# Kernel optimization log

Hardware: AMD Instinct MI355X
Metric: run time of the kernel (lower is better)

## Reference

```python
import jax, jax.numpy as jnp
import numpy as np

B, N, F0 = 256, 256, 128
LAYER_SIZES = [128, 128, 128]


def setup_inputs() -> dict:
    key = jax.random.key(0)
    ks = jax.random.split(key, 10)
    x = jax.random.normal(ks[0], (B, N, F0), dtype=jnp.float32)
    adj = jax.random.uniform(ks[1], (B, N, N), dtype=jnp.float32)
    adj = 0.5 * (adj + jnp.swapaxes(adj, -1, -2))  # symmetric weighted adjacency
    f0, f1, f2 = LAYER_SIZES
    W1 = jax.random.normal(ks[2], (f0, f1), dtype=jnp.float32) / np.sqrt(f0)
    b1 = jnp.zeros((f1,), dtype=jnp.float32)
    W2 = jax.random.normal(ks[3], (f1, f2), dtype=jnp.float32) / np.sqrt(f1)
    b2 = jnp.zeros((f2,), dtype=jnp.float32)
    Wr = jax.random.normal(ks[4], (2 * f2, f2), dtype=jnp.float32) / np.sqrt(2 * f2)
    br = jnp.zeros((f2,), dtype=jnp.float32)
    return {"x": x, "adj": adj, "W1": W1, "b1": b1, "W2": W2, "b2": b2, "Wr": Wr, "br": br}


def _normalize_adj(adj):
    # DenseGCNConv: set self-loops (diag=1), then D^{-1/2} (A+I) D^{-1/2} with deg clamped to >=1
    n = adj.shape[-1]
    eye = jnp.eye(n, dtype=adj.dtype)
    a = adj * (1.0 - eye) + eye
    d = jnp.maximum(a.sum(axis=-1), 1.0) ** -0.5  # [B, N]
    return d[..., :, None] * a * d[..., None, :]


def reference(x, adj, W1, b1, W2, b2, Wr, br):
    a = _normalize_adj(adj)  # same adj for both layers; normalization is identical per layer
    h = jnp.einsum("bnm,bmf->bnf", a, x @ W1) + b1  # DenseGCNConv layer 1
    h = jnp.einsum("bnm,bmf->bnf", a, h @ W2) + b2  # DenseGCNConv layer 2
    pooled = jnp.concatenate([h.mean(axis=1), h.max(axis=1)], axis=-1)  # [B, 2F]
    return pooled @ Wr + br  # [B, F]
```

## Files before the change

### kernel.cpp

```cpp
#include <hip/hip_runtime.h>
#include <cstddef>


typedef __attribute__((ext_vector_type(8))) short short8;
typedef __attribute__((ext_vector_type(4))) float f32x4;

static __device__ __forceinline__ unsigned short f2bf(float f) {
  unsigned int u = __float_as_uint(f);
  u += 0x7FFFu + ((u >> 16) & 1u);
  return (unsigned short)(u >> 16);
}

static __device__ __forceinline__ f32x4 mfma16(short8 a, short8 b, f32x4 c) {
  return __builtin_amdgcn_mfma_f32_16x16x32_bf16(a, b, c, 0, 0, 0);
}

static __device__ __forceinline__ short8 load_bfrag(const float* p) {
  float4 u = *reinterpret_cast<const float4*>(p);
  float4 v = *reinterpret_cast<const float4*>(p + 4);
  short8 f;
  f[0] = (short)f2bf(u.x); f[1] = (short)f2bf(u.y);
  f[2] = (short)f2bf(u.z); f[3] = (short)f2bf(u.w);
  f[4] = (short)f2bf(v.x); f[5] = (short)f2bf(v.y);
  f[6] = (short)f2bf(v.z); f[7] = (short)f2bf(v.w);
  return f;
}

static __device__ __forceinline__ int byteT(int f, int k) {
  return ((f << 9) + (k << 1)) ^ ((f & 7) << 4);
}
static __device__ __forceinline__ int byteH(int n, int k) {
  return ((n << 8) + (k << 1)) ^ ((n & 7) << 4);
}

__global__ __launch_bounds__(64) void k_packW2(
    const float* __restrict__ W1, const float* __restrict__ W2,
    unsigned short* __restrict__ P1, unsigned short* __restrict__ P2) {
  const float* W = (blockIdx.x < 32) ? W1 : W2;
  unsigned short* P = (blockIdx.x < 32) ? P1 : P2;
  const int bb = blockIdx.x & 31;
  const int ks = bb >> 3;
  const int r = bb & 7;
  const int l = threadIdx.x;
  const int col = r * 16 + (l & 15);
  const int k0 = ks * 32 + ((l >> 4) << 3);
  short8 frag;
  #pragma unroll
  for (int j = 0; j < 8; ++j)
    frag[j] = (short)f2bf(W[(size_t)(k0 + j) * 128 + col]);
  *reinterpret_cast<short8*>(P + ((size_t)((ks * 8 + r) * 64 + l)) * 8) = frag;
}

__global__ __launch_bounds__(512) void k_fused(
    const float* __restrict__ adj, const float* __restrict__ x,
    const unsigned short* __restrict__ W1p, const unsigned short* __restrict__ W2p,
    const float* __restrict__ b1, const float* __restrict__ b2,
    const float* __restrict__ Wr, const float* __restrict__ br,
    unsigned short* __restrict__ Abf, float* __restrict__ out) {
  __shared__ __align__(16) char bufA[65536];
  __shared__ __align__(16) char bufB[65536];
  __shared__ float dinv_s[256];

  const int b = blockIdx.x;
  const int tid = threadIdx.x;
  const int w = tid >> 6;
  const int l = tid & 63;
  const int l15 = l & 15;
  const int khalf = (l >> 4) << 3;
  const int qbase = (l >> 4) << 2;

  {
    const int cq = tid & 63;
    const int rg = tid >> 6;
    const int c0 = cq << 2;
    const float* adjb = adj + ((size_t)b << 16);
    unsigned short* Ab = Abf + ((size_t)b << 16);
    float sx = 0.f, sy = 0.f, sz = 0.f, sw = 0.f;
    #pragma unroll 4
    for (int i = 0; i < 32; ++i) {
      const int r = (rg << 5) + i;
      float4 v = *reinterpret_cast<const float4*>(adjb + r * 256 + c0);
      v.x = (r == c0 + 0) ? 1.0f : v.x;
      v.y = (r == c0 + 1) ? 1.0f : v.y;
      v.z = (r == c0 + 2) ? 1.0f : v.z;
      v.w = (r == c0 + 3) ? 1.0f : v.w;
      sx += v.x; sy += v.y; sz += v.z; sw += v.w;
      ushort4 o;
      o.x = f2bf(v.x); o.y = f2bf(v.y); o.z = f2bf(v.z); o.w = f2bf(v.w);
      *reinterpret_cast<ushort4*>(Ab + r * 256 + c0) = o;
    }
    float* red = reinterpret_cast<float*>(bufB);
    float4 st; st.x = sx; st.y = sy; st.z = sz; st.w = sw;
    *reinterpret_cast<float4*>(red + (rg << 8) + c0) = st;
  }
  __syncthreads();
  if (tid < 256) {
    const float* red = reinterpret_cast<const float*>(bufB);
    float s = 0.f;
    #pragma unroll
    for (int g = 0; g < 8; ++g) s += red[(g << 8) + tid];
    dinv_s[tid] = rsqrtf(fmaxf(s, 1.0f));
  }
  __syncthreads();

  {
    const short8* Wf = reinterpret_cast<const short8*>(W1p);
    for (int p = 0; p < 2; ++p) {
      const int m = (p << 7) + (w << 4) + l15;
      const float* xr = x + ((((size_t)b << 8) + m) << 7);
      f32x4 acc[8];
      #pragma unroll
      for (int r = 0; r < 8; ++r) acc[r] = (f32x4)(0.0f);
      #pragma unroll
      for (int ks = 0; ks < 4; ++ks) {
        short8 bf = load_bfrag(xr + (ks << 5) + khalf);
        #pragma unroll
        for (int r = 0; r < 8; ++r)
          acc[r] = mfma16(Wf[((ks << 3) + r) * 64 + l], bf, acc[r]);
      }
      const float sc = dinv_s[m];
      #pragma unroll
      for (int r = 0; r < 8; ++r) {
        #pragma unroll
        for (int q = 0; q < 4; ++q) {
          const int f = (r << 4) + qbase + q;
          *reinterpret_cast<unsigned short*>(bufA + byteT(f, m)) =
              f2bf(acc[r][q] * sc);
        }
      }
    }
  }
  __syncthreads();

  {
    const unsigned short* Ab = Abf + ((size_t)b << 16);
    const int n0w = w << 5;
    float bs[8];
    #pragma unroll
    for (int c = 0; c < 8; ++c) bs[c] = b1[(c << 4) + l15];
    f32x4 acc[2][8];
    #pragma unroll
    for (int rt = 0; rt < 2; ++rt)
      #pragma unroll
      for (int c = 0; c < 8; ++c) acc[rt][c] = (f32x4)(0.0f);
    #pragma unroll
    for (int ks = 0; ks < 8; ++ks) {
      const int k0 = (ks << 5) + khalf;
      short8 a0 = *reinterpret_cast<const short8*>(Ab + (size_t)(n0w + l15) * 256 + k0);
      short8 a1 = *reinterpret_cast<const short8*>(Ab + (size_t)(n0w + 16 + l15) * 256 + k0);
      #pragma unroll
      for (int c = 0; c < 8; ++c) {
        short8 bf = *reinterpret_cast<const short8*>(bufA + byteT((c << 4) + l15, k0));
        acc[0][c] = mfma16(a0, bf, acc[0][c]);
        acc[1][c] = mfma16(a1, bf, acc[1][c]);
      }
    }
    #pragma unroll
    for (int rt = 0; rt < 2; ++rt) {
      #pragma unroll
      for (int q = 0; q < 4; ++q) {
        const int n = n0w + (rt << 4) + qbase + q;
        const float dv = dinv_s[n];
        #pragma unroll
        for (int c = 0; c < 8; ++c) {
          const int f = (c << 4) + l15;
          *reinterpret_cast<unsigned short*>(bufB + byteH(n, f)) =
              f2bf(acc[rt][c][q] * dv + bs[c]);
        }
      }
    }
  }
  __syncthreads();

  {
    const short8* Wf = reinterpret_cast<const short8*>(W2p);
    for (int p = 0; p < 2; ++p) {
      const int m = (p << 7) + (w << 4) + l15;
      f32x4 acc[8];
      #pragma unroll
      for (int r = 0; r < 8; ++r) acc[r] = (f32x4)(0.0f);
      #pragma unroll
      for (int ks = 0; ks < 4; ++ks) {
        const int kk = (ks << 5) + khalf;
        short8 bf = *reinterpret_cast<const short8*>(bufB + byteH(m, kk));
        #pragma unroll
        for (int r = 0; r < 8; ++r)
          acc[r] = mfma16(Wf[((ks << 3) + r) * 64 + l], bf, acc[r]);
      }
      const float sc = dinv_s[m];
      #pragma unroll
      for (int r = 0; r < 8; ++r) {
        #pragma unroll
        for (int q = 0; q < 4; ++q) {
          const int f = (r << 4) + qbase + q;
          *reinterpret_cast<unsigned short*>(bufA + byteT(f, m)) =
              f2bf(acc[r][q] * sc);
        }
      }
    }
  }
  __syncthreads();

  {
    const unsigned short* Ab = Abf + ((size_t)b << 16);
    const int n0w = w << 5;
    float bs[8];
    #pragma unroll
    for (int c = 0; c < 8; ++c) bs[c] = b2[(c << 4) + l15];
    f32x4 acc[2][8];
    #pragma unroll
    for (int rt = 0; rt < 2; ++rt)
      #pragma unroll
      for (int c = 0; c < 8; ++c) acc[rt][c] = (f32x4)(0.0f);
    #pragma unroll
    for (int ks = 0; ks < 8; ++ks) {
      const int k0 = (ks << 5) + khalf;
      short8 a0 = *reinterpret_cast<const short8*>(Ab + (size_t)(n0w + l15) * 256 + k0);
      short8 a1 = *reinterpret_cast<const short8*>(Ab + (size_t)(n0w + 16 + l15) * 256 + k0);
      #pragma unroll
      for (int c = 0; c < 8; ++c) {
        short8 bf = *reinterpret_cast<const short8*>(bufA + byteT((c << 4) + l15, k0));
        acc[0][c] = mfma16(a0, bf, acc[0][c]);
        acc[1][c] = mfma16(a1, bf, acc[1][c]);
      }
    }
    float psum[8], pmax[8];
    #pragma unroll
    for (int c = 0; c < 8; ++c) { psum[c] = 0.0f; pmax[c] = -1e30f; }
    #pragma unroll
    for (int rt = 0; rt < 2; ++rt) {
      #pragma unroll
      for (int q = 0; q < 4; ++q) {
        const int n = n0w + (rt << 4) + qbase + q;
        const float dv = dinv_s[n];
        #pragma unroll
        for (int c = 0; c < 8; ++c) {
          const float v = acc[rt][c][q] * dv + bs[c];
          psum[c] += v;
          pmax[c] = fmaxf(pmax[c], v);
        }
      }
    }
    #pragma unroll
    for (int c = 0; c < 8; ++c) {
      psum[c] += __shfl_xor(psum[c], 16);
      pmax[c] = fmaxf(pmax[c], __shfl_xor(pmax[c], 16));
      psum[c] += __shfl_xor(psum[c], 32);
      pmax[c] = fmaxf(pmax[c], __shfl_xor(pmax[c], 32));
    }
    float* lds_sum = reinterpret_cast<float*>(bufB);
    float* lds_max = lds_sum + 1024;
    float* pooled = lds_max + 1024;
    if (l < 16) {
      #pragma unroll
      for (int c = 0; c < 8; ++c) {
        lds_sum[(w << 7) + (c << 4) + l] = psum[c];
        lds_max[(w << 7) + (c << 4) + l] = pmax[c];
      }
    }
    __syncthreads();
    if (tid < 128) {
      float s = 0.0f, m = -1e30f;
      #pragma unroll
      for (int ww = 0; ww < 8; ++ww) {
        s += lds_sum[(ww << 7) + tid];
        m = fmaxf(m, lds_max[(ww << 7) + tid]);
      }
      pooled[tid] = s * (1.0f / 256.0f);
      pooled[128 + tid] = m;
    }
    __syncthreads();
    if (tid < 128) {
      float o0 = 0.f, o1 = 0.f, o2 = 0.f, o3 = 0.f;
      for (int i = 0; i < 256; i += 4) {
        o0 = fmaf(pooled[i + 0], Wr[(i + 0) * 128 + tid], o0);
        o1 = fmaf(pooled[i + 1], Wr[(i + 1) * 128 + tid], o1);
        o2 = fmaf(pooled[i + 2], Wr[(i + 2) * 128 + tid], o2);
        o3 = fmaf(pooled[i + 3], Wr[(i + 3) * 128 + tid], o3);
      }
      out[(b << 7) + tid] = ((o0 + o1) + (o2 + o3)) + br[tid];
    }
  }
}

extern "C" void kernel_launch(void* const* d_in, const int* in_sizes, int n_in,
                              void* d_out, int out_size, void* d_ws, size_t ws_size,
                              hipStream_t stream) {
  const float* x   = (const float*)d_in[0];
  const float* adj = (const float*)d_in[1];
  const float* W1  = (const float*)d_in[2];
  const float* b1  = (const float*)d_in[3];
  const float* W2  = (const float*)d_in[4];
  const float* b2  = (const float*)d_in[5];
  const float* Wr  = (const float*)d_in[6];
  const float* br  = (const float*)d_in[7];
  float* out = (float*)d_out;

  char* ws = (char*)d_ws;
  unsigned short* Abf = (unsigned short*)(ws);
  unsigned short* W1p = (unsigned short*)(ws + 33554432);
  unsigned short* W2p = (unsigned short*)(ws + 33587200);

  k_packW2<<<64, 64, 0, stream>>>(W1, W2, W1p, W2p);
  k_fused<<<256, 512, 0, stream>>>(adj, x, W1p, W2p, b1, b2, Wr, br, Abf, out);
}
```

Measured before the change: 63.78 us.

## Double block to 1024 threads, overlap x loads with adjacency pass

```diff
diff --git a/kernel.cpp b/kernel.cpp
--- a/kernel.cpp
+++ b/kernel.cpp
@@ -13,17 +13,6 @@
 
 static __device__ __forceinline__ f32x4 mfma16(short8 a, short8 b, f32x4 c) {
   return __builtin_amdgcn_mfma_f32_16x16x32_bf16(a, b, c, 0, 0, 0);
-}
-
-static __device__ __forceinline__ short8 load_bfrag(const float* p) {
-  float4 u = *reinterpret_cast<const float4*>(p);
-  float4 v = *reinterpret_cast<const float4*>(p + 4);
-  short8 f;
-  f[0] = (short)f2bf(u.x); f[1] = (short)f2bf(u.y);
-  f[2] = (short)f2bf(u.z); f[3] = (short)f2bf(u.w);
-  f[4] = (short)f2bf(v.x); f[5] = (short)f2bf(v.y);
-  f[6] = (short)f2bf(v.z); f[7] = (short)f2bf(v.w);
-  return f;
 }
 
 static __device__ __forceinline__ int byteT(int f, int k) {
@@ -51,7 +40,7 @@
   *reinterpret_cast<short8*>(P + ((size_t)((ks * 8 + r) * 64 + l)) * 8) = frag;
 }
 
-__global__ __launch_bounds__(512) void k_fused(
+__global__ __launch_bounds__(1024, 4) void k_fused(
     const float* __restrict__ adj, const float* __restrict__ x,
     const unsigned short* __restrict__ W1p, const unsigned short* __restrict__ W2p,
     const float* __restrict__ b1, const float* __restrict__ b2,
@@ -68,18 +57,27 @@
   const int l15 = l & 15;
   const int khalf = (l >> 4) << 3;
   const int qbase = (l >> 4) << 2;
-
-  {
-    const int cq = tid & 63;
-    const int rg = tid >> 6;
-    const int c0 = cq << 2;
+  const int m = (w << 4) + l15;
+
+  float4 xraw[8];
+  {
+    const float* xr = x + ((((size_t)b << 8) + m) << 7);
+    #pragma unroll
+    for (int ks = 0; ks < 4; ++ks) {
+      xraw[2 * ks]     = *reinterpret_cast<const float4*>(xr + (ks << 5) + khalf);
+      xraw[2 * ks + 1] = *reinterpret_cast<const float4*>(xr + (ks << 5) + khalf + 4);
+    }
+  }
+
+  {
+    const int c0 = l << 2;
     const float* adjb = adj + ((size_t)b << 16);
     unsigned short* Ab = Abf + ((size_t)b << 16);
     float sx = 0.f, sy = 0.f, sz = 0.f, sw = 0.f;
     #pragma unroll 4
-    for (int i = 0; i < 32; ++i) {
-      const int r = (rg << 5) + i;
-      float4 v = *reinterpret_cast<const float4*>(adjb + r * 256 + c0);
+    for (int i = 0; i < 16; ++i) {
+      const int r = (w << 4) + i;
+      float4 v = *reinterpret_cast<const float4*>(adjb + (r << 8) + c0);
       v.x = (r == c0 + 0) ? 1.0f : v.x;
       v.y = (r == c0 + 1) ? 1.0f : v.y;
       v.z = (r == c0 + 2) ? 1.0f : v.z;
@@ -87,158 +85,141 @@
       sx += v.x; sy += v.y; sz += v.z; sw += v.w;
       ushort4 o;
       o.x = f2bf(v.x); o.y = f2bf(v.y); o.z = f2bf(v.z); o.w = f2bf(v.w);
-      *reinterpret_cast<ushort4*>(Ab + r * 256 + c0) = o;
-    }
-    float* red = reinterpret_cast<float*>(bufB);
+      *reinterpret_cast<ushort4*>(Ab + (r << 8) + c0) = o;
+    }
+    float* red = reinterpret_cast<float*>(bufA);
     float4 st; st.x = sx; st.y = sy; st.z = sz; st.w = sw;
-    *reinterpret_cast<float4*>(red + (rg << 8) + c0) = st;
+    *reinterpret_cast<float4*>(red + (w << 8) + c0) = st;
+  }
+
+  f32x4 acc1[8];
+  #pragma unroll
+  for (int r = 0; r < 8; ++r) acc1[r] = (f32x4)(0.0f);
+  {
+    const short8* Wf = reinterpret_cast<const short8*>(W1p);
+    #pragma unroll
+    for (int ks = 0; ks < 4; ++ks) {
+      const float4 u = xraw[2 * ks], v = xraw[2 * ks + 1];
+      short8 bf;
+      bf[0] = (short)f2bf(u.x); bf[1] = (short)f2bf(u.y);
+      bf[2] = (short)f2bf(u.z); bf[3] = (short)f2bf(u.w);
+      bf[4] = (short)f2bf(v.x); bf[5] = (short)f2bf(v.y);
+      bf[6] = (short)f2bf(v.z); bf[7] = (short)f2bf(v.w);
+      #pragma unroll
+      for (int r = 0; r < 8; ++r)
+        acc1[r] = mfma16(Wf[((ks << 3) + r) * 64 + l], bf, acc1[r]);
+    }
   }
   __syncthreads();
   if (tid < 256) {
-    const float* red = reinterpret_cast<const float*>(bufB);
+    const float* red = reinterpret_cast<const float*>(bufA);
     float s = 0.f;
     #pragma unroll
-    for (int g = 0; g < 8; ++g) s += red[(g << 8) + tid];
+    for (int g = 0; g < 16; ++g) s += red[(g << 8) + tid];
     dinv_s[tid] = rsqrtf(fmaxf(s, 1.0f));
   }
   __syncthreads();
 
   {
-    const short8* Wf = reinterpret_cast<const short8*>(W1p);
-    for (int p = 0; p < 2; ++p) {
-      const int m = (p << 7) + (w << 4) + l15;
-      const float* xr = x + ((((size_t)b << 8) + m) << 7);
-      f32x4 acc[8];
-      #pragma unroll
-      for (int r = 0; r < 8; ++r) acc[r] = (f32x4)(0.0f);
-      #pragma unroll
-      for (int ks = 0; ks < 4; ++ks) {
-        short8 bf = load_bfrag(xr + (ks << 5) + khalf);
-        #pragma unroll
-        for (int r = 0; r < 8; ++r)
-          acc[r] = mfma16(Wf[((ks << 3) + r) * 64 + l], bf, acc[r]);
-      }
-      const float sc = dinv_s[m];
-      #pragma unroll
-      for (int r = 0; r < 8; ++r) {
-        #pragma unroll
-        for (int q = 0; q < 4; ++q) {
-          const int f = (r << 4) + qbase + q;
-          *reinterpret_cast<unsigned short*>(bufA + byteT(f, m)) =
-              f2bf(acc[r][q] * sc);
-        }
-      }
-    }
-  }
-  __syncthreads();
-
-  {
-    const unsigned short* Ab = Abf + ((size_t)b << 16);
-    const int n0w = w << 5;
-    float bs[8];
-    #pragma unroll
-    for (int c = 0; c < 8; ++c) bs[c] = b1[(c << 4) + l15];
-    f32x4 acc[2][8];
-    #pragma unroll
-    for (int rt = 0; rt < 2; ++rt)
-      #pragma unroll
-      for (int c = 0; c < 8; ++c) acc[rt][c] = (f32x4)(0.0f);
+    const float sc = dinv_s[m];
+    #pragma unroll
+    for (int r = 0; r < 8; ++r) {
+      #pragma unroll
+      for (int q = 0; q < 4; ++q) {
+        const int f = (r << 4) + qbase + q;
+        *reinterpret_cast<unsigned short*>(bufA + byteT(f, m)) =
+            f2bf(acc1[r][q] * sc);
+      }
+    }
+  }
+  __syncthreads();
+
+  const unsigned short* Ab = Abf + ((size_t)b << 16);
+  const int n0w = w << 4;
+  {
+    f32x4 acc[8];
+    #pragma unroll
+    for (int c = 0; c < 8; ++c) acc[c] = (f32x4)(0.0f);
     #pragma unroll
     for (int ks = 0; ks < 8; ++ks) {
       const int k0 = (ks << 5) + khalf;
       short8 a0 = *reinterpret_cast<const short8*>(Ab + (size_t)(n0w + l15) * 256 + k0);
-      short8 a1 = *reinterpret_cast<const short8*>(Ab + (size_t)(n0w + 16 + l15) * 256 + k0);
       #pragma unroll
       for (int c = 0; c < 8; ++c) {
         short8 bf = *reinterpret_cast<const short8*>(bufA + byteT((c << 4) + l15, k0));
-        acc[0][c] = mfma16(a0, bf, acc[0][c]);
-        acc[1][c] = mfma16(a1, bf, acc[1][c]);
-      }
-    }
-    #pragma unroll
-    for (int rt = 0; rt < 2; ++rt) {
+        acc[c] = mfma16(a0, bf, acc[c]);
+      }
+    }
+    float bs[8];
+    #pragma unroll
+    for (int c = 0; c < 8; ++c) bs[c] = b1[(c << 4) + l15];
+    #pragma unroll
+    for (int q = 0; q < 4; ++q) {
+      const int n = n0w + qbase + q;
+      const float dv = dinv_s[n];
+      #pragma unroll
+      for (int c = 0; c < 8; ++c)
+        *reinterpret_cast<unsigned short*>(bufB + byteH(n, (c << 4) + l15)) =
+            f2bf(acc[c][q] * dv + bs[c]);
+    }
+  }
+  __syncthreads();
+
+  {
+    const short8* Wf = reinterpret_cast<const short8*>(W2p);
+    f32x4 acc[8];
+    #pragma unroll
+    for (int r = 0; r < 8; ++r) acc[r] = (f32x4)(0.0f);
+    #pragma unroll
+    for (int ks = 0; ks < 4; ++ks) {
+      const int kk = (ks << 5) + khalf;
+      short8 hf = *reinterpret_cast<const short8*>(bufB + byteH(m, kk));
+      #pragma unroll
+      for (int r = 0; r < 8; ++r)
+        acc[r] = mfma16(Wf[((ks << 3) + r) * 64 + l], hf, acc[r]);
+    }
+    const float sc = dinv_s[m];
+    #pragma unroll
+    for (int r = 0; r < 8; ++r) {
       #pragma unroll
       for (int q = 0; q < 4; ++q) {
-        const int n = n0w + (rt << 4) + qbase + q;
-        const float dv = dinv_s[n];
-        #pragma unroll
-        for (int c = 0; c < 8; ++c) {
-          const int f = (c << 4) + l15;
-          *reinterpret_cast<unsigned short*>(bufB + byteH(n, f)) =
-              f2bf(acc[rt][c][q] * dv + bs[c]);
-        }
-      }
-    }
-  }
-  __syncthreads();
-
-  {
-    const short8* Wf = reinterpret_cast<const short8*>(W2p);
-    for (int p = 0; p < 2; ++p) {
-      const int m = (p << 7) + (w << 4) + l15;
-      f32x4 acc[8];
-      #pragma unroll
-      for (int r = 0; r < 8; ++r) acc[r] = (f32x4)(0.0f);
-      #pragma unroll
-      for (int ks = 0; ks < 4; ++ks) {
-        const int kk = (ks << 5) + khalf;
-        short8 bf = *reinterpret_cast<const short8*>(bufB + byteH(m, kk));
-        #pragma unroll
-        for (int r = 0; r < 8; ++r)
-          acc[r] = mfma16(Wf[((ks << 3) + r) * 64 + l], bf, acc[r]);
-      }
-      const float sc = dinv_s[m];
-      #pragma unroll
-      for (int r = 0; r < 8; ++r) {
-        #pragma unroll
-        for (int q = 0; q < 4; ++q) {
-          const int f = (r << 4) + qbase + q;
-          *reinterpret_cast<unsigned short*>(bufA + byteT(f, m)) =
-              f2bf(acc[r][q] * sc);
-        }
-      }
-    }
-  }
-  __syncthreads();
-
-  {
-    const unsigned short* Ab = Abf + ((size_t)b << 16);
-    const int n0w = w << 5;
-    float bs[8];
-    #pragma unroll
-    for (int c = 0; c < 8; ++c) bs[c] = b2[(c << 4) + l15];
-    f32x4 acc[2][8];
-    #pragma unroll
-    for (int rt = 0; rt < 2; ++rt)
-      #pragma unroll
-      for (int c = 0; c < 8; ++c) acc[rt][c] = (f32x4)(0.0f);
+        const int f = (r << 4) + qbase + q;
+        *reinterpret_cast<unsigned short*>(bufA + byteT(f, m)) =
+            f2bf(acc[r][q] * sc);
+      }
+    }
+  }
+  __syncthreads();
+
+  {
+    f32x4 acc[8];
+    #pragma unroll
+    for (int c = 0; c < 8; ++c) acc[c] = (f32x4)(0.0f);
     #pragma unroll
     for (int ks = 0; ks < 8; ++ks) {
       const int k0 = (ks << 5) + khalf;
       short8 a0 = *reinterpret_cast<const short8*>(Ab + (size_t)(n0w + l15) * 256 + k0);
-      short8 a1 = *reinterpret_cast<const short8*>(Ab + (size_t)(n0w + 16 + l15) * 256 + k0);
       #pragma unroll
       for (int c = 0; c < 8; ++c) {
         short8 bf = *reinterpret_cast<const short8*>(bufA + byteT((c << 4) + l15, k0));
-        acc[0][c] = mfma16(a0, bf, acc[0][c]);
-        acc[1][c] = mfma16(a1, bf, acc[1][c]);
-      }
-    }
-    float psum[8], pmax[8];
-    #pragma unroll
-    for (int c = 0; c < 8; ++c) { psum[c] = 0.0f; pmax[c] = -1e30f; }
-    #pragma unroll
-    for (int rt = 0; rt < 2; ++rt) {
-      #pragma unroll
-      for (int q = 0; q < 4; ++q) {
-        const int n = n0w + (rt << 4) + qbase + q;
-        const float dv = dinv_s[n];
-        #pragma unroll
-        for (int c = 0; c < 8; ++c) {
-          const float v = acc[rt][c][q] * dv + bs[c];
-          psum[c] += v;
-          pmax[c] = fmaxf(pmax[c], v);
-        }
+        acc[c] = mfma16(a0, bf, acc[c]);
+      }
+    }
+    float bs[8], psum[8], pmax[8];
+    #pragma unroll
+    for (int c = 0; c < 8; ++c) {
+      bs[c] = b2[(c << 4) + l15];
+      psum[c] = 0.0f; pmax[c] = -1e30f;
+    }
+    #pragma unroll
+    for (int q = 0; q < 4; ++q) {
+      const int n = n0w + qbase + q;
+      const float dv = dinv_s[n];
+      #pragma unroll
+      for (int c = 0; c < 8; ++c) {
+        const float v = acc[c][q] * dv + bs[c];
+        psum[c] += v;
+        pmax[c] = fmaxf(pmax[c], v);
       }
     }
     #pragma unroll
@@ -249,8 +230,9 @@
       pmax[c] = fmaxf(pmax[c], __shfl_xor(pmax[c], 32));
     }
     float* lds_sum = reinterpret_cast<float*>(bufB);
-    float* lds_max = lds_sum + 1024;
-    float* pooled = lds_max + 1024;
+    float* lds_max = lds_sum + 2048;
+    float* pooled  = lds_max + 2048;
+    float* rp      = pooled + 256;
     if (l < 16) {
       #pragma unroll
       for (int c = 0; c < 8; ++c) {
@@ -260,26 +242,33 @@
     }
     __syncthreads();
     if (tid < 128) {
-      float s = 0.0f, m = -1e30f;
-      #pragma unroll
-      for (int ww = 0; ww < 8; ++ww) {
-        s += lds_sum[(ww << 7) + tid];
-        m = fmaxf(m, lds_max[(ww << 7) + tid]);
-      }
+      float s = 0.0f;
+      #pragma unroll
+      for (int ww = 0; ww < 16; ++ww) s += lds_sum[(ww << 7) + tid];
       pooled[tid] = s * (1.0f / 256.0f);
-      pooled[128 + tid] = m;
+    } else if (tid < 256) {
+      const int f = tid & 127;
+      float mx = -1e30f;
+      #pragma unroll
+      for (int ww = 0; ww < 16; ++ww) mx = fmaxf(mx, lds_max[(ww << 7) + f]);
+      pooled[128 + f] = mx;
     }
     __syncthreads();
-    if (tid < 128) {
-      float o0 = 0.f, o1 = 0.f, o2 = 0.f, o3 = 0.f;
-      for (int i = 0; i < 256; i += 4) {
-        o0 = fmaf(pooled[i + 0], Wr[(i + 0) * 128 + tid], o0);
-        o1 = fmaf(pooled[i + 1], Wr[(i + 1) * 128 + tid], o1);
-        o2 = fmaf(pooled[i + 2], Wr[(i + 2) * 128 + tid], o2);
-        o3 = fmaf(pooled[i + 3], Wr[(i + 3) * 128 + tid], o3);
-      }
-      out[(b << 7) + tid] = ((o0 + o1) + (o2 + o3)) + br[tid];
-    }
+    if (tid < 512) {
+      const int f = tid & 127, part = tid >> 7;
+      const int base = part << 6;
+      float o0 = 0.f, o1 = 0.f;
+      #pragma unroll 4
+      for (int i = 0; i < 64; i += 2) {
+        o0 = fmaf(pooled[base + i],     Wr[(base + i) * 128 + f],     o0);
+        o1 = fmaf(pooled[base + i + 1], Wr[(base + i + 1) * 128 + f], o1);
+      }
+      rp[(part << 7) + f] = o0 + o1;
+    }
+    __syncthreads();
+    if (tid < 128)
+      out[(b << 7) + tid] =
+          ((rp[tid] + rp[128 + tid]) + (rp[256 + tid] + rp[384 + tid])) + br[tid];
   }
 }
 
@@ -302,5 +291,5 @@
   unsigned short* W2p = (unsigned short*)(ws + 33587200);
 
   k_packW2<<<64, 64, 0, stream>>>(W1, W2, W1p, W2p);
-  k_fused<<<256, 512, 0, stream>>>(adj, x, W1p, W2p, b1, b2, Wr, br, Abf, out);
-}
+  k_fused<<<256, 1024, 0, stream>>>(adj, x, W1p, W2p, b1, b2, Wr, br, Abf, out);
+}
```

Measured after the change: 74.02 us. +16.0%, slower.
